# Kernel tuning notes

Hardware: AMD Instinct MI355X
Metric: run time of the kernel (lower is better)

The kernel has to match this reference:

```python
import jax, jax.numpy as jnp
import numpy as np

NUM_HEADS = 16
KEY_DIM = 64
D_MODEL = NUM_HEADS * KEY_DIM
BATCH = 2
SEQ = 2048


def _rope_tables(seq_len, dim, dtype):
    # matches RotaryPositionalEmbedding: inv_freq = exp(arange(0,dim,2) * (-ln(10000)/dim))
    pos = jnp.arange(seq_len, dtype=dtype)                      # [S]
    inv_freq = jnp.exp(jnp.arange(0, dim, 2, dtype=dtype) * (-np.log(10000.0) / dim))  # [D/2]
    angles = pos[:, None] * inv_freq[None, :]                   # [S, D/2]
    return jnp.sin(angles), jnp.cos(angles)


def _apply_rope(x, sin, cos):
    # x: [B, S, H, D]; sin/cos: [S, D/2] broadcast over batch and heads
    sin = sin[None, :, None, :]
    cos = cos[None, :, None, :]
    x1, x2 = jnp.split(x, 2, axis=-1)
    return jnp.concatenate([cos * x1 - sin * x2, sin * x1 + cos * x2], axis=-1)


def setup_inputs() -> dict:
    key = jax.random.key(0)
    ks = jax.random.split(key, 5)
    s = 1.0 / np.sqrt(D_MODEL)
    return {
        "inputs": jax.random.normal(ks[0], (BATCH, SEQ, D_MODEL), jnp.float32),
        "Wq": jax.random.normal(ks[1], (D_MODEL, D_MODEL), jnp.float32) * s,
        "bq": jnp.zeros((D_MODEL,), jnp.float32),
        "Wk": jax.random.normal(ks[2], (D_MODEL, D_MODEL), jnp.float32) * s,
        "bk": jnp.zeros((D_MODEL,), jnp.float32),
        "Wv": jax.random.normal(ks[3], (D_MODEL, D_MODEL), jnp.float32) * s,
        "bv": jnp.zeros((D_MODEL,), jnp.float32),
        "Wo": jax.random.normal(ks[4], (D_MODEL, D_MODEL), jnp.float32) * s,
        "bo": jnp.zeros((D_MODEL,), jnp.float32),
    }


def reference(inputs, Wq, bq, Wk, bk, Wv, bv, Wo, bo):
    B, S, _ = inputs.shape
    # QKV projections, split into heads: [B, S, H, Dk]
    q = (inputs @ Wq + bq).reshape(B, S, NUM_HEADS, KEY_DIM)
    k = (inputs @ Wk + bk).reshape(B, S, NUM_HEADS, KEY_DIM)
    v = (inputs @ Wv + bv).reshape(B, S, NUM_HEADS, KEY_DIM)
    # rotary embedding on q/k (per-head dim = KEY_DIM)
    sin, cos = _rope_tables(S, KEY_DIM, inputs.dtype)
    q = _apply_rope(q, sin, cos)
    k = _apply_rope(k, sin, cos)
    # attention: [B, H, S, S]
    scores = jnp.einsum("bshd,bthd->bhst", q, k) / jnp.sqrt(
        jnp.asarray(KEY_DIM, inputs.dtype))
    weights = jax.nn.softmax(scores, axis=-1)  # dropout inactive (training=False)
    ctx = jnp.einsum("bhst,bthd->bshd", weights, v).reshape(B, S, D_MODEL)
    return ctx @ Wo + bo
```

## Files before the change

### kernel.cpp

```cpp
#include <hip/hip_runtime.h>
#include <math.h>

#define NH 16
#define KD 64
#define DMODEL 1024
#define BATCH 2
#define SEQ 2048
#define MROWS (BATCH*SEQ)

typedef float f32x4 __attribute__((ext_vector_type(4)));
typedef __bf16 bf16x8 __attribute__((ext_vector_type(8)));

__device__ __forceinline__ unsigned short f2bf(float x) {
    union { float f; unsigned u; } a; a.f = x;
    unsigned r = a.u + 0x7fffu + ((a.u >> 16) & 1u);
    return (unsigned short)(r >> 16);
}
__device__ __forceinline__ unsigned cvt_pk_bf16(float lo, float hi) {
    unsigned r;
    asm("v_cvt_pk_bf16_f32 %0, %1, %2" : "=v"(r) : "v"(lo), "v"(hi));
    return r;
}
__device__ __forceinline__ float exp2_hw(float x) {
    float r;
    asm("v_exp_f32 %0, %1" : "=v"(r) : "v"(x));
    return r;
}

__device__ __forceinline__ void gl2lds16(const void* gsrc, void* ldst) {
    __builtin_amdgcn_global_load_lds(
        (const __attribute__((address_space(1))) void*)gsrc,
        (__attribute__((address_space(3))) void*)ldst, 16, 0, 0);
}

__global__ __launch_bounds__(256) void k_prep(const float* __restrict__ x,
                                              const float* __restrict__ W0,
                                              const float* __restrict__ W1,
                                              const float* __restrict__ W2,
                                              const float* __restrict__ W3,
                                              float* __restrict__ sin_t,
                                              float* __restrict__ cos_t,
                                              unsigned short* __restrict__ xh,
                                              unsigned short* __restrict__ Th) {
    __shared__ float L[64][65];
    const int bid = blockIdx.x;
    const int tid = threadIdx.x;
    if (bid < 256) {
        int idx = bid * 256 + tid;
        int s = idx >> 5, i = idx & 31;
        float invf = expf((float)(2 * i) * (-logf(10000.0f) / (float)KD));
        float ang = (float)s * invf;
        sin_t[idx] = sinf(ang);
        cos_t[idx] = cosf(ang);
        return;
    }
    if (bid < 4352) {
        int idx = (bid - 256) * 256 + tid;
        float4 v = reinterpret_cast<const float4*>(x)[idx];
        ushort4 h;
        h.x = f2bf(v.x); h.y = f2bf(v.y); h.z = f2bf(v.z); h.w = f2bf(v.w);
        reinterpret_cast<ushort4*>(xh)[idx] = h;
        return;
    }
    int r = bid - 4352;
    int z = r >> 8;
    int rr = r & 255;
    const int n0 = (rr & 15) * 64, k0 = (rr >> 4) * 64;
    const float* W = (z == 0) ? W0 : (z == 1) ? W1 : (z == 2) ? W2 : W3;
    const size_t zoff = (size_t)z * DMODEL * DMODEL;
#pragma unroll
    for (int it = 0; it < 4; ++it) {
        int idx = tid + it * 256;
        int rw = idx >> 4;
        int c4 = (idx & 15) * 4;
        float4 v = *reinterpret_cast<const float4*>(&W[(size_t)(k0 + rw) * DMODEL + n0 + c4]);
        L[rw][c4 + 0] = v.x; L[rw][c4 + 1] = v.y; L[rw][c4 + 2] = v.z; L[rw][c4 + 3] = v.w;
    }
    __syncthreads();
    int rn = tid >> 2;
    int ks = (tid & 3) * 16;
#pragma unroll
    for (int g = 0; g < 4; ++g) {
        ushort4 h;
        h.x = f2bf(L[ks + g * 4 + 0][rn]);
        h.y = f2bf(L[ks + g * 4 + 1][rn]);
        h.z = f2bf(L[ks + g * 4 + 2][rn]);
        h.w = f2bf(L[ks + g * 4 + 3][rn]);
        size_t o = zoff + (size_t)(n0 + rn) * DMODEL + k0 + ks + g * 4;
        *reinterpret_cast<ushort4*>(&Th[o]) = h;
    }
}

__global__ __launch_bounds__(256) void k_mgemm_qkv(const unsigned short* __restrict__ Ah_g,
                                                   const unsigned short* __restrict__ Wp,
                                                   const float* __restrict__ bq,
                                                   const float* __restrict__ bk,
                                                   const float* __restrict__ bv,
                                                   unsigned short* __restrict__ qh_,
                                                   unsigned short* __restrict__ kh_,
                                                   unsigned short* __restrict__ vth,
                                                   const float* __restrict__ sin_t,
                                                   const float* __restrict__ cos_t) {
    __shared__ unsigned short Ah[2][128 * 64];
    __shared__ unsigned short Bh[2][3][64 * 64];
    const int tid = threadIdx.x;
    const int lane = tid & 63;
    const int w = tid >> 6;

    int bid = blockIdx.x;
    int wg = (bid & 7) * 64 + (bid >> 3);
    const int m0 = (wg >> 4) * 128;
    const int n0 = (wg & 15) * 64;
    const size_t WE = (size_t)DMODEL * DMODEL;

    size_t a_goff[4]; int a_ldst[4];
#pragma unroll
    for (int it = 0; it < 4; ++it) {
        int off = it * 4096 + w * 1024 + lane * 16;
        int row = off >> 7;
        int pg = (off >> 4) & 7;
        int lg = pg ^ (row & 7);
        a_goff[it] = (size_t)(m0 + row) * DMODEL + lg * 8;
        a_ldst[it] = it * 2048 + w * 512;
    }
    size_t b_goff[2]; int b_ldst[2];
#pragma unroll
    for (int it = 0; it < 2; ++it) {
        int off = it * 4096 + w * 1024 + lane * 16;
        int row = off >> 7;
        int pg = (off >> 4) & 7;
        int lg = pg ^ (row & 7);
        b_goff[it] = (size_t)(n0 + row) * DMODEL + lg * 8;
        b_ldst[it] = it * 2048 + w * 512;
    }

    int aoff[2][2], boff[4][2];
#pragma unroll
    for (int mf = 0; mf < 2; ++mf)
#pragma unroll
        for (int ks = 0; ks < 2; ++ks) {
            int row = w * 32 + mf * 16 + (lane & 15);
            int g = ks * 4 + (lane >> 4);
            aoff[mf][ks] = row * 64 + ((g ^ (row & 7)) * 8);
        }
#pragma unroll
    for (int nf = 0; nf < 4; ++nf)
#pragma unroll
        for (int ks = 0; ks < 2; ++ks) {
            int row = nf * 16 + (lane & 15);
            int g = ks * 4 + (lane >> 4);
            boff[nf][ks] = row * 64 + ((g ^ (row & 7)) * 8);
        }

    f32x4 acc[3][2][4];
#pragma unroll
    for (int z = 0; z < 3; ++z)
#pragma unroll
        for (int mf = 0; mf < 2; ++mf)
#pragma unroll
            for (int nf = 0; nf < 4; ++nf) acc[z][mf][nf] = (f32x4){0.f, 0.f, 0.f, 0.f};

#define STAGEG(BUF, KT) do {                                                  \
        int k0_ = (KT) * 64;                                                  \
        gl2lds16(Ah_g + a_goff[0] + k0_, &Ah[BUF][a_ldst[0]]);                \
        gl2lds16(Ah_g + a_goff[1] + k0_, &Ah[BUF][a_ldst[1]]);                \
        gl2lds16(Ah_g + a_goff[2] + k0_, &Ah[BUF][a_ldst[2]]);                \
        gl2lds16(Ah_g + a_goff[3] + k0_, &Ah[BUF][a_ldst[3]]);                \
        gl2lds16(Wp + 0 * WE + b_goff[0] + k0_, &Bh[BUF][0][b_ldst[0]]);      \
        gl2lds16(Wp + 0 * WE + b_goff[1] + k0_, &Bh[BUF][0][b_ldst[1]]);      \
        gl2lds16(Wp + 1 * WE + b_goff[0] + k0_, &Bh[BUF][1][b_ldst[0]]);      \
        gl2lds16(Wp + 1 * WE + b_goff[1] + k0_, &Bh[BUF][1][b_ldst[1]]);      \
        gl2lds16(Wp + 2 * WE + b_goff[0] + k0_, &Bh[BUF][2][b_ldst[0]]);      \
        gl2lds16(Wp + 2 * WE + b_goff[1] + k0_, &Bh[BUF][2][b_ldst[1]]);      \
    } while (0)

    STAGEG(0, 0);

    for (int kt = 0; kt < 16; ++kt) {
        const int cur = kt & 1;
        asm volatile("s_waitcnt vmcnt(0)" ::: "memory");
        __builtin_amdgcn_s_barrier();
        if (kt < 15) STAGEG(cur ^ 1, kt + 1);
#pragma unroll
        for (int ks = 0; ks < 2; ++ks) {
            bf16x8 ah[2];
#pragma unroll
            for (int mf = 0; mf < 2; ++mf)
                ah[mf] = *reinterpret_cast<const bf16x8*>(&Ah[cur][aoff[mf][ks]]);
#pragma unroll
            for (int z = 0; z < 3; ++z) {
                bf16x8 bh[4];
#pragma unroll
                for (int nf = 0; nf < 4; ++nf)
                    bh[nf] = *reinterpret_cast<const bf16x8*>(&Bh[cur][z][boff[nf][ks]]);
#pragma unroll
                for (int mf = 0; mf < 2; ++mf)
#pragma unroll
                    for (int nf = 0; nf < 4; ++nf)
                        acc[z][mf][nf] = __builtin_amdgcn_mfma_f32_16x16x32_bf16(ah[mf], bh[nf], acc[z][mf][nf], 0, 0, 0);
            }
        }
    }
#undef STAGEG

    const int c = lane & 15;
    const int rq = lane >> 4;
    float bvq[4], bvk[4], bvv[4];
#pragma unroll
    for (int nf = 0; nf < 4; ++nf) {
        bvq[nf] = bq[n0 + nf * 16 + c];
        bvk[nf] = bk[n0 + nf * 16 + c];
        bvv[nf] = bv[n0 + nf * 16 + c];
    }

#pragma unroll
    for (int mf = 0; mf < 2; ++mf) {
        int mbase = m0 + w * 32 + mf * 16 + rq * 4;
#pragma unroll
        for (int z = 0; z < 2; ++z) {
            const float* bb_ = (z == 0) ? bvq : bvk;
            unsigned short* Ohi = (z == 0) ? qh_ : kh_;
#pragma unroll
            for (int r2 = 0; r2 < 4; ++r2) {
                int m = mbase + r2;
                int srow = m & (SEQ - 1);
                float x0 = acc[z][mf][0][r2] + bb_[0];
                float x1 = acc[z][mf][1][r2] + bb_[1];
                float x2 = acc[z][mf][2][r2] + bb_[2];
                float x3 = acc[z][mf][3][r2] + bb_[3];
                float s0 = sin_t[srow * 32 + c],      c0 = cos_t[srow * 32 + c];
                float s1 = sin_t[srow * 32 + 16 + c], c1 = cos_t[srow * 32 + 16 + c];
                float o0 = c0 * x0 - s0 * x2;
                float o2 = s0 * x0 + c0 * x2;
                float o1 = c1 * x1 - s1 * x3;
                float o3 = s1 * x1 + c1 * x3;
                if (z == 0) {
                    const float qs = 0.18033688011112042f;
                    o0 *= qs; o1 *= qs; o2 *= qs; o3 *= qs;
                }
                float ov[4] = { o0, o1, o2, o3 };
                size_t base = (size_t)m * DMODEL + n0 + c;
#pragma unroll
                for (int nf = 0; nf < 4; ++nf)
                    Ohi[base + nf * 16] = f2bf(ov[nf]);
            }
        }
        {
            int bb = mbase >> 11;
            int s = mbase & (SEQ - 1);
            int h = n0 >> 6;
#pragma unroll
            for (int nf = 0; nf < 4; ++nf) {
                ushort4 h4;
                float v0 = acc[2][mf][nf][0] + bvv[nf];
                float v1 = acc[2][mf][nf][1] + bvv[nf];
                float v2 = acc[2][mf][nf][2] + bvv[nf];
                float v3 = acc[2][mf][nf][3] + bvv[nf];
                h4.x = f2bf(v0); h4.y = f2bf(v1); h4.z = f2bf(v2); h4.w = f2bf(v3);
                int d = nf * 16 + c;
                size_t o = ((size_t)((bb * NH + h) * KD + d)) * SEQ + s;
                *reinterpret_cast<ushort4*>(&vth[o]) = h4;
            }
        }
    }
}

__global__ __launch_bounds__(256) void k_mgemm_o(const unsigned short* __restrict__ Ah_g,
                                                 const unsigned short* __restrict__ Bh_g,
                                                 const float* __restrict__ bias,
                                                 float* __restrict__ Cf) {
    __shared__ unsigned short Ah[2][128 * 64];
    __shared__ unsigned short Bh[2][64 * 64];
    const int tid = threadIdx.x;
    const int lane = tid & 63;
    const int w = tid >> 6;

    int bid = blockIdx.x;
    int wg = (bid & 7) * 64 + (bid >> 3);
    const int m0 = (wg >> 4) * 128;
    const int n0 = (wg & 15) * 64;

    size_t a_goff[4]; int a_ldst[4];
#pragma unroll
    for (int it = 0; it < 4; ++it) {
        int off = it * 4096 + w * 1024 + lane * 16;
        int row = off >> 7;
        int pg = (off >> 4) & 7;
        int lg = pg ^ (row & 7);
        a_goff[it] = (size_t)(m0 + row) * DMODEL + lg * 8;
        a_ldst[it] = it * 2048 + w * 512;
    }
    size_t b_goff[2]; int b_ldst[2];
#pragma unroll
    for (int it = 0; it < 2; ++it) {
        int off = it * 4096 + w * 1024 + lane * 16;
        int row = off >> 7;
        int pg = (off >> 4) & 7;
        int lg = pg ^ (row & 7);
        b_goff[it] = (size_t)(n0 + row) * DMODEL + lg * 8;
        b_ldst[it] = it * 2048 + w * 512;
    }

    int aoff[2][2], boff[4][2];
#pragma unroll
    for (int mf = 0; mf < 2; ++mf)
#pragma unroll
        for (int ks = 0; ks < 2; ++ks) {
            int row = w * 32 + mf * 16 + (lane & 15);
            int g = ks * 4 + (lane >> 4);
            aoff[mf][ks] = row * 64 + ((g ^ (row & 7)) * 8);
        }
#pragma unroll
    for (int nf = 0; nf < 4; ++nf)
#pragma unroll
        for (int ks = 0; ks < 2; ++ks) {
            int row = nf * 16 + (lane & 15);
            int g = ks * 4 + (lane >> 4);
            boff[nf][ks] = row * 64 + ((g ^ (row & 7)) * 8);
        }

    f32x4 acc[2][4];
#pragma unroll
    for (int mf = 0; mf < 2; ++mf)
#pragma unroll
        for (int nf = 0; nf < 4; ++nf) acc[mf][nf] = (f32x4){0.f, 0.f, 0.f, 0.f};

#define STAGEG(BUF, KT) do {                                                  \
        int k0_ = (KT) * 64;                                                  \
        gl2lds16(Ah_g + a_goff[0] + k0_, &Ah[BUF][a_ldst[0]]);                \
        gl2lds16(Ah_g + a_goff[1] + k0_, &Ah[BUF][a_ldst[1]]);                \
        gl2lds16(Ah_g + a_goff[2] + k0_, &Ah[BUF][a_ldst[2]]);                \
        gl2lds16(Ah_g + a_goff[3] + k0_, &Ah[BUF][a_ldst[3]]);                \
        gl2lds16(Bh_g + b_goff[0] + k0_, &Bh[BUF][b_ldst[0]]);                \
        gl2lds16(Bh_g + b_goff[1] + k0_, &Bh[BUF][b_ldst[1]]);                \
    } while (0)

    STAGEG(0, 0);

    for (int kt = 0; kt < 16; ++kt) {
        const int cur = kt & 1;
        asm volatile("s_waitcnt vmcnt(0)" ::: "memory");
        __builtin_amdgcn_s_barrier();
        if (kt < 15) STAGEG(cur ^ 1, kt + 1);
#pragma unroll
        for (int ks = 0; ks < 2; ++ks) {
            bf16x8 ah[2], bh[4];
#pragma unroll
            for (int mf = 0; mf < 2; ++mf)
                ah[mf] = *reinterpret_cast<const bf16x8*>(&Ah[cur][aoff[mf][ks]]);
#pragma unroll
            for (int nf = 0; nf < 4; ++nf)
                bh[nf] = *reinterpret_cast<const bf16x8*>(&Bh[cur][boff[nf][ks]]);
#pragma unroll
            for (int mf = 0; mf < 2; ++mf)
#pragma unroll
                for (int nf = 0; nf < 4; ++nf)
                    acc[mf][nf] = __builtin_amdgcn_mfma_f32_16x16x32_bf16(ah[mf], bh[nf], acc[mf][nf], 0, 0, 0);
        }
    }
#undef STAGEG

    const int c = lane & 15;
    const int rq = lane >> 4;
    float bv[4];
#pragma unroll
    for (int nf = 0; nf < 4; ++nf) bv[nf] = bias[n0 + nf * 16 + c];
#pragma unroll
    for (int mf = 0; mf < 2; ++mf) {
        int mbase = m0 + w * 32 + mf * 16 + rq * 4;
#pragma unroll
        for (int nf = 0; nf < 4; ++nf)
#pragma unroll
            for (int r = 0; r < 4; ++r)
                Cf[(size_t)(mbase + r) * DMODEL + n0 + nf * 16 + c] = acc[mf][nf][r] + bv[nf];
    }
}

__global__ __launch_bounds__(256) void k_attn(const unsigned short* __restrict__ qhi,
                                              const unsigned short* __restrict__ khi,
                                              const unsigned short* __restrict__ vthi,
                                              unsigned short* __restrict__ ch) {
    __shared__ unsigned short Kh[2][64 * 64];
    __shared__ unsigned short Vh[3][64 * 64];
    __shared__ unsigned short Ps[4][32 * 64];

    const int tid  = threadIdx.x;
    const int lane = tid & 63;
    const int w    = tid >> 6;

    int bid = blockIdx.x;
    int wg  = (bid & 7) * 64 + (bid >> 3);
    const int qt = wg & 15;
    const int h  = (wg >> 4) & 15;
    const int b  = wg >> 8;
    const int q0 = qt * 128;

    bf16x8 qf[2][2];
#pragma unroll
    for (int mf = 0; mf < 2; ++mf)
#pragma unroll
        for (int ks = 0; ks < 2; ++ks) {
            int row = q0 + w * 32 + mf * 16 + (lane & 15);
            int d = ks * 32 + (lane >> 4) * 8;
            qf[mf][ks] = *reinterpret_cast<const bf16x8*>(
                qhi + ((size_t)(b * SEQ + row) * NH + h) * KD + d);
        }

    size_t gK[2], gV[2]; int ld_[2];
#pragma unroll
    for (int it = 0; it < 2; ++it) {
        int off = it * 4096 + tid * 16;
        int row = off >> 7;
        int pg = (off >> 4) & 7;
        int lg = pg ^ (row & 7);
        gK[it] = ((size_t)(b * SEQ + row) * NH + h) * KD + lg * 8;
        gV[it] = ((size_t)(b * NH + h) * KD + row) * SEQ + lg * 8;
        ld_[it] = it * 2048 + w * 512;
    }

    f32x4 acc[2][4];
    float l_part[2] = { 0.f, 0.f };
#pragma unroll
    for (int mf = 0; mf < 2; ++mf)
#pragma unroll
        for (int nf = 0; nf < 4; ++nf) acc[mf][nf] = (f32x4){0.f, 0.f, 0.f, 0.f};

#define STAGE(KB, VB, TT) do {                                               \
        size_t kadv = (size_t)(TT) * 64 * NH * KD;                           \
        size_t vadv = (size_t)(TT) * 64;                                     \
        gl2lds16(khi  + gK[0] + kadv, &Kh[KB][ld_[0]]);                      \
        gl2lds16(khi  + gK[1] + kadv, &Kh[KB][ld_[1]]);                      \
        gl2lds16(vthi + gV[0] + vadv, &Vh[VB][ld_[0]]);                      \
        gl2lds16(vthi + gV[1] + vadv, &Vh[VB][ld_[1]]);                      \
    } while (0)

#define PV_STEP(VSRC) do {                                                   \
        _Pragma("unroll")                                                    \
        for (int ks = 0; ks < 2; ++ks) {                                     \
            bf16x8 pa[2];                                                    \
            _Pragma("unroll")                                                \
            for (int mf = 0; mf < 2; ++mf) {                                 \
                int prow = mf * 16 + (lane & 15);                            \
                int aoff = prow * 64 + (((ks * 4 + (lane >> 4)) ^ (prow & 7)) * 8); \
                pa[mf] = *reinterpret_cast<const bf16x8*>(&Ps[w][aoff]);     \
            }                                                                \
            _Pragma("unroll")                                                \
            for (int nf = 0; nf < 4; ++nf) {                                 \
                int drow = nf * 16 + (lane & 15);                            \
                int voff = drow * 64 + (((ks * 4 + (lane >> 4)) ^ (drow & 7)) * 8); \
                bf16x8 vf = *reinterpret_cast<const bf16x8*>(&Vh[VSRC][voff]); \
                _Pragma("unroll")                                            \
                for (int mf = 0; mf < 2; ++mf)                               \
                    acc[mf][nf] = __builtin_amdgcn_mfma_f32_16x16x32_bf16(pa[mf], vf, acc[mf][nf], 0, 0, 0); \
            }                                                                \
        }                                                                    \
    } while (0)

    STAGE(0, 0, 0);

    int vnext = 1;
    int vprev = 2;

    for (int t = 0; t < 32; ++t) {
        const int ck = t & 1;
        asm volatile("s_waitcnt vmcnt(0)" ::: "memory");
        __builtin_amdgcn_s_barrier();
        if (t < 31) STAGE(ck ^ 1, vnext, t + 1);

        __builtin_amdgcn_s_setprio(1);
        f32x4 s[2][4];
#pragma unroll
        for (int mf = 0; mf < 2; ++mf)
#pragma unroll
            for (int nf = 0; nf < 4; ++nf) s[mf][nf] = (f32x4){0.f, 0.f, 0.f, 0.f};
#pragma unroll
        for (int nf = 0; nf < 4; ++nf) {
#pragma unroll
            for (int ks = 0; ks < 2; ++ks) {
                int trow = nf * 16 + (lane & 15);
                int koff = trow * 64 + (((ks * 4 + (lane >> 4)) ^ (trow & 7)) * 8);
                bf16x8 kf = *reinterpret_cast<const bf16x8*>(&Kh[ck][koff]);
#pragma unroll
                for (int mf = 0; mf < 2; ++mf)
                    s[mf][nf] = __builtin_amdgcn_mfma_f32_16x16x32_bf16(kf, qf[mf][ks], s[mf][nf], 0, 0, 0);
            }
        }
        if (t > 0) PV_STEP(vprev);
        __builtin_amdgcn_s_setprio(0);

#pragma unroll
        for (int mf = 0; mf < 2; ++mf) {
            int qloc = mf * 16 + (lane & 15);
#pragma unroll
            for (int nf = 0; nf < 4; ++nf) {
                float p0 = exp2_hw(s[mf][nf][0]);
                float p1 = exp2_hw(s[mf][nf][1]);
                float p2 = exp2_hw(s[mf][nf][2]);
                float p3 = exp2_hw(s[mf][nf][3]);
                l_part[mf] += (p0 + p1) + (p2 + p3);
                unsigned w01 = cvt_pk_bf16(p0, p1);
                unsigned w23 = cvt_pk_bf16(p2, p3);
                int tb = nf * 16 + (lane >> 4) * 4;
                int phys = tb ^ ((qloc & 7) << 3);
                *reinterpret_cast<uint2*>(&Ps[w][qloc * 64 + phys]) = make_uint2(w01, w23);
            }
        }

        vnext = (vnext == 2) ? 0 : vnext + 1;
        vprev = (vprev == 2) ? 0 : vprev + 1;
    }

    PV_STEP(vprev);
#undef PV_STEP
#undef STAGE

#pragma unroll
    for (int mf = 0; mf < 2; ++mf) {
        l_part[mf] += __shfl_xor(l_part[mf], 16);
        l_part[mf] += __shfl_xor(l_part[mf], 32);
    }
#pragma unroll
    for (int mf = 0; mf < 2; ++mf) {
#pragma unroll
        for (int r = 0; r < 4; ++r) {
            float lsum = __shfl(l_part[mf], (lane >> 4) * 4 + r);
            float inv = 1.0f / lsum;
            int qg = q0 + w * 32 + mf * 16 + (lane >> 4) * 4 + r;
#pragma unroll
            for (int nf = 0; nf < 4; ++nf) {
                int d = nf * 16 + (lane & 15);
                float val = acc[mf][nf][r] * inv;
                ch[((size_t)(b * SEQ + qg) * NH + h) * KD + d] = f2bf(val);
            }
        }
    }
}

extern "C" void kernel_launch(void* const* d_in, const int* in_sizes, int n_in,
                              void* d_out, int out_size, void* d_ws, size_t ws_size,
                              hipStream_t stream) {
    const float* x  = (const float*)d_in[0];
    const float* Wq = (const float*)d_in[1];
    const float* bq = (const float*)d_in[2];
    const float* Wk = (const float*)d_in[3];
    const float* bk = (const float*)d_in[4];
    const float* Wv = (const float*)d_in[5];
    const float* bv = (const float*)d_in[6];
    const float* Wo = (const float*)d_in[7];
    const float* bo = (const float*)d_in[8];
    float* out = (float*)d_out;

    const size_t NE = (size_t)MROWS * DMODEL;
    const size_t WE = (size_t)DMODEL * DMODEL;
    float* ws    = (float*)d_ws;
    float* sin_t = ws;
    float* cos_t = sin_t + SEQ * 32;
    unsigned short* p = (unsigned short*)(cos_t + SEQ * 32);
    unsigned short* xh   = p; p += NE;
    unsigned short* qh_  = p; p += NE;
    unsigned short* kh_  = p; p += NE;
    unsigned short* vth  = p; p += NE;
    unsigned short* wth  = p; p += 4 * WE;
    unsigned short* ctxh = xh;

    k_prep<<<5376, 256, 0, stream>>>(x, Wq, Wk, Wv, Wo, sin_t, cos_t, xh, wth);

    k_mgemm_qkv<<<512, 256, 0, stream>>>(xh, wth, bq, bk, bv, qh_, kh_, vth, sin_t, cos_t);

    k_attn<<<512, 256, 0, stream>>>(qh_, kh_, vth, ctxh);

    k_mgemm_o<<<512, 256, 0, stream>>>(ctxh, wth + 3 * WE, bo, out);
}
```

Measured before the change: 113.8 us.

## Switch attention to 32x32x16 MFMA and keep P in registers via permlane32 swap

```diff
diff --git a/kernel.cpp b/kernel.cpp
--- a/kernel.cpp
+++ b/kernel.cpp
@@ -9,6 +9,7 @@
 #define MROWS (BATCH*SEQ)
 
 typedef float f32x4 __attribute__((ext_vector_type(4)));
+typedef float f32x16 __attribute__((ext_vector_type(16)));
 typedef __bf16 bf16x8 __attribute__((ext_vector_type(8)));
 
 __device__ __forceinline__ unsigned short f2bf(float x) {
@@ -382,7 +383,6 @@
                                               unsigned short* __restrict__ ch) {
     __shared__ unsigned short Kh[2][64 * 64];
     __shared__ unsigned short Vh[3][64 * 64];
-    __shared__ unsigned short Ps[4][32 * 64];
 
     const int tid  = threadIdx.x;
     const int lane = tid & 63;
@@ -395,16 +395,16 @@
     const int b  = wg >> 8;
     const int q0 = qt * 128;
 
-    bf16x8 qf[2][2];
-#pragma unroll
-    for (int mf = 0; mf < 2; ++mf)
-#pragma unroll
-        for (int ks = 0; ks < 2; ++ks) {
-            int row = q0 + w * 32 + mf * 16 + (lane & 15);
-            int d = ks * 32 + (lane >> 4) * 8;
-            qf[mf][ks] = *reinterpret_cast<const bf16x8*>(
-                qhi + ((size_t)(b * SEQ + row) * NH + h) * KD + d);
-        }
+    const int l31 = lane & 31;
+    const int lh  = lane >> 5;
+
+    bf16x8 qf[4];
+#pragma unroll
+    for (int ks = 0; ks < 4; ++ks) {
+        int row = q0 + w * 32 + l31;
+        qf[ks] = *reinterpret_cast<const bf16x8*>(
+            qhi + ((size_t)(b * SEQ + row) * NH + h) * KD + ks * 16 + lh * 8);
+    }
 
     size_t gK[2], gV[2]; int ld_[2];
 #pragma unroll
@@ -418,12 +418,22 @@
         ld_[it] = it * 2048 + w * 512;
     }
 
-    f32x4 acc[2][4];
-    float l_part[2] = { 0.f, 0.f };
-#pragma unroll
-    for (int mf = 0; mf < 2; ++mf)
-#pragma unroll
-        for (int nf = 0; nf < 4; ++nf) acc[mf][nf] = (f32x4){0.f, 0.f, 0.f, 0.f};
+    int foff[2][4];
+#pragma unroll
+    for (int tb = 0; tb < 2; ++tb)
+#pragma unroll
+        for (int ks = 0; ks < 4; ++ks)
+            foff[tb][ks] = (tb * 32 + l31) * 64 + (((ks * 2 + lh) ^ (lane & 7)) * 8);
+
+    f32x16 acc[2];
+#pragma unroll
+    for (int db = 0; db < 2; ++db)
+#pragma unroll
+        for (int r = 0; r < 16; ++r) acc[db][r] = 0.f;
+    float l_part = 0.f;
+
+    unsigned paw[4][4];
+    union U8 { unsigned u[4]; bf16x8 v; };
 
 #define STAGE(KB, VB, TT) do {                                               \
         size_t kadv = (size_t)(TT) * 64 * NH * KD;                           \
@@ -436,22 +446,13 @@
 
 #define PV_STEP(VSRC) do {                                                   \
         _Pragma("unroll")                                                    \
-        for (int ks = 0; ks < 2; ++ks) {                                     \
-            bf16x8 pa[2];                                                    \
+        for (int db = 0; db < 2; ++db) {                                     \
             _Pragma("unroll")                                                \
-            for (int mf = 0; mf < 2; ++mf) {                                 \
-                int prow = mf * 16 + (lane & 15);                            \
-                int aoff = prow * 64 + (((ks * 4 + (lane >> 4)) ^ (prow & 7)) * 8); \
-                pa[mf] = *reinterpret_cast<const bf16x8*>(&Ps[w][aoff]);     \
-            }                                                                \
-            _Pragma("unroll")                                                \
-            for (int nf = 0; nf < 4; ++nf) {                                 \
-                int drow = nf * 16 + (lane & 15);                            \
-                int voff = drow * 64 + (((ks * 4 + (lane >> 4)) ^ (drow & 7)) * 8); \
-                bf16x8 vf = *reinterpret_cast<const bf16x8*>(&Vh[VSRC][voff]); \
-                _Pragma("unroll")                                            \
-                for (int mf = 0; mf < 2; ++mf)                               \
-                    acc[mf][nf] = __builtin_amdgcn_mfma_f32_16x16x32_bf16(pa[mf], vf, acc[mf][nf], 0, 0, 0); \
+            for (int ks = 0; ks < 4; ++ks) {                                 \
+                bf16x8 vf = *reinterpret_cast<const bf16x8*>(&Vh[VSRC][foff[db][ks]]); \
+                U8 pa; pa.u[0] = paw[ks][0]; pa.u[1] = paw[ks][1];           \
+                pa.u[2] = paw[ks][2]; pa.u[3] = paw[ks][3];                  \
+                acc[db] = __builtin_amdgcn_mfma_f32_32x32x16_bf16(pa.v, vf, acc[db], 0, 0, 0); \
             }                                                                \
         }                                                                    \
     } while (0)
@@ -468,41 +469,40 @@
         if (t < 31) STAGE(ck ^ 1, vnext, t + 1);
 
         __builtin_amdgcn_s_setprio(1);
-        f32x4 s[2][4];
-#pragma unroll
-        for (int mf = 0; mf < 2; ++mf)
-#pragma unroll
-            for (int nf = 0; nf < 4; ++nf) s[mf][nf] = (f32x4){0.f, 0.f, 0.f, 0.f};
-#pragma unroll
-        for (int nf = 0; nf < 4; ++nf) {
-#pragma unroll
-            for (int ks = 0; ks < 2; ++ks) {
-                int trow = nf * 16 + (lane & 15);
-                int koff = trow * 64 + (((ks * 4 + (lane >> 4)) ^ (trow & 7)) * 8);
-                bf16x8 kf = *reinterpret_cast<const bf16x8*>(&Kh[ck][koff]);
-#pragma unroll
-                for (int mf = 0; mf < 2; ++mf)
-                    s[mf][nf] = __builtin_amdgcn_mfma_f32_16x16x32_bf16(kf, qf[mf][ks], s[mf][nf], 0, 0, 0);
+        f32x16 s[2];
+#pragma unroll
+        for (int tb = 0; tb < 2; ++tb) {
+#pragma unroll
+            for (int r = 0; r < 16; ++r) s[tb][r] = 0.f;
+#pragma unroll
+            for (int ks = 0; ks < 4; ++ks) {
+                bf16x8 kf = *reinterpret_cast<const bf16x8*>(&Kh[ck][foff[tb][ks]]);
+                s[tb] = __builtin_amdgcn_mfma_f32_32x32x16_bf16(kf, qf[ks], s[tb], 0, 0, 0);
             }
         }
         if (t > 0) PV_STEP(vprev);
         __builtin_amdgcn_s_setprio(0);
 
 #pragma unroll
-        for (int mf = 0; mf < 2; ++mf) {
-            int qloc = mf * 16 + (lane & 15);
-#pragma unroll
-            for (int nf = 0; nf < 4; ++nf) {
-                float p0 = exp2_hw(s[mf][nf][0]);
-                float p1 = exp2_hw(s[mf][nf][1]);
-                float p2 = exp2_hw(s[mf][nf][2]);
-                float p3 = exp2_hw(s[mf][nf][3]);
-                l_part[mf] += (p0 + p1) + (p2 + p3);
-                unsigned w01 = cvt_pk_bf16(p0, p1);
-                unsigned w23 = cvt_pk_bf16(p2, p3);
-                int tb = nf * 16 + (lane >> 4) * 4;
-                int phys = tb ^ ((qloc & 7) << 3);
-                *reinterpret_cast<uint2*>(&Ps[w][qloc * 64 + phys]) = make_uint2(w01, w23);
+        for (int tb = 0; tb < 2; ++tb) {
+            float e[16];
+#pragma unroll
+            for (int r = 0; r < 16; ++r) {
+                e[r] = exp2_hw(s[tb][r]);
+                l_part += e[r];
+            }
+#pragma unroll
+            for (int half = 0; half < 2; ++half) {
+                unsigned pk01 = cvt_pk_bf16(e[half * 8 + 0], e[half * 8 + 1]);
+                unsigned pk23 = cvt_pk_bf16(e[half * 8 + 2], e[half * 8 + 3]);
+                unsigned pk45 = cvt_pk_bf16(e[half * 8 + 4], e[half * 8 + 5]);
+                unsigned pk67 = cvt_pk_bf16(e[half * 8 + 6], e[half * 8 + 7]);
+                asm volatile("v_permlane32_swap_b32 %0, %1" : "+v"(pk01), "+v"(pk45));
+                asm volatile("v_permlane32_swap_b32 %0, %1" : "+v"(pk23), "+v"(pk67));
+                paw[tb * 2 + half][0] = pk01;
+                paw[tb * 2 + half][1] = pk23;
+                paw[tb * 2 + half][2] = pk45;
+                paw[tb * 2 + half][3] = pk67;
             }
         }
 
@@ -514,24 +514,21 @@
 #undef PV_STEP
 #undef STAGE
 
-#pragma unroll
-    for (int mf = 0; mf < 2; ++mf) {
-        l_part[mf] += __shfl_xor(l_part[mf], 16);
-        l_part[mf] += __shfl_xor(l_part[mf], 32);
-    }
-#pragma unroll
-    for (int mf = 0; mf < 2; ++mf) {
-#pragma unroll
-        for (int r = 0; r < 4; ++r) {
-            float lsum = __shfl(l_part[mf], (lane >> 4) * 4 + r);
-            float inv = 1.0f / lsum;
-            int qg = q0 + w * 32 + mf * 16 + (lane >> 4) * 4 + r;
-#pragma unroll
-            for (int nf = 0; nf < 4; ++nf) {
-                int d = nf * 16 + (lane & 15);
-                float val = acc[mf][nf][r] * inv;
-                ch[((size_t)(b * SEQ + qg) * NH + h) * KD + d] = f2bf(val);
-            }
+    l_part += __shfl_xor(l_part, 32);
+    float linv[16];
+#pragma unroll
+    for (int r = 0; r < 16; ++r) {
+        int q = (r & 3) + 8 * (r >> 2) + 4 * lh;
+        linv[r] = 1.0f / __shfl(l_part, q);
+    }
+#pragma unroll
+    for (int db = 0; db < 2; ++db) {
+#pragma unroll
+        for (int r = 0; r < 16; ++r) {
+            int q = (r & 3) + 8 * (r >> 2) + 4 * lh;
+            int qg = q0 + w * 32 + q;
+            int d = db * 32 + l31;
+            ch[((size_t)(b * SEQ + qg) * NH + h) * KD + d] = f2bf(acc[db][r] * linv[r]);
         }
     }
 }
```

After: 111.3 us. -2.2%, faster.
